# Optimization experiments

Hardware: AMD Instinct MI355X
Metric: run time of the kernel (lower is better)

The kernel has to match this reference:

```python
import jax, jax.numpy as jnp
import numpy as np

B, N, C = 16, 1025, 1024
H, D = 16, 64          # num_heads, head_dim
NPT = 1                # num_prefix_tokens
EPS = 1e-6
SCALE = D ** -0.5


def layer_norm(x, g, b, eps=EPS):
    mu = jnp.mean(x, axis=-1, keepdims=True)
    var = jnp.mean(jnp.square(x - mu), axis=-1, keepdims=True)
    return (x - mu) * jax.lax.rsqrt(var + eps) * g + b


def rot(x):
    # interleaved rotate-half: out[..., ::2] = -x[..., 1::2]; out[..., 1::2] = x[..., ::2]
    x2 = x.reshape(*x.shape[:-1], -1, 2)
    return jnp.stack([-x2[..., 1], x2[..., 0]], axis=-1).reshape(x.shape)


def apply_rot_embed_cat(x, emb):
    # emb: (N_spatial, 2*D) = [sin | cos]
    sin_emb, cos_emb = jnp.split(emb, 2, axis=-1)
    return x * cos_emb + rot(x) * sin_emb


def setup_inputs() -> dict:
    key = jax.random.key(0)
    ks = jax.random.split(key, 12)
    s = 0.02
    return {
        "x": jax.random.normal(ks[0], (B, N, C), jnp.float32),
        "rope": jax.random.normal(ks[1], (N - NPT, 2 * D), jnp.float32),
        "qkv_w": jax.random.normal(ks[2], (3 * C, C), jnp.float32) * s,
        "q_bias": jax.random.normal(ks[3], (C,), jnp.float32) * s,
        "k_bias": jnp.zeros((C,), jnp.float32),  # registered buffer, always zero
        "v_bias": jax.random.normal(ks[4], (C,), jnp.float32) * s,
        "qn_g": jnp.ones((D,), jnp.float32),
        "qn_b": jnp.zeros((D,), jnp.float32),
        "kn_g": jnp.ones((D,), jnp.float32),
        "kn_b": jnp.zeros((D,), jnp.float32),
        "norm_g": jnp.ones((C,), jnp.float32),
        "norm_b": jnp.zeros((C,), jnp.float32),
        "proj_w": jax.random.normal(ks[5], (C, C), jnp.float32) * s,
        "proj_b": jnp.zeros((C,), jnp.float32),
    }


def reference(x, rope, qkv_w, q_bias, k_bias, v_bias, qn_g, qn_b, kn_g, kn_b,
              norm_g, norm_b, proj_w, proj_b):
    b, n, c = x.shape
    qkv_bias = jnp.concatenate([q_bias, k_bias, v_bias])
    qkv = jnp.einsum('bnc,oc->bno', x, qkv_w) + qkv_bias          # (B,N,3C)
    qkv = qkv.reshape(b, n, 3, H, D).transpose(2, 0, 3, 1, 4)     # (3,B,H,N,D)
    q, k, v = qkv[0], qkv[1], qkv[2]
    # per-head QK layernorm over head_dim
    q = layer_norm(q, qn_g, qn_b)
    k = layer_norm(k, kn_g, kn_b)
    # RoPE on spatial tokens only (prefix tokens excluded)
    q = jnp.concatenate([q[:, :, :NPT], apply_rot_embed_cat(q[:, :, NPT:], rope)], axis=2)
    k = jnp.concatenate([k[:, :, :NPT], apply_rot_embed_cat(k[:, :, NPT:], rope)], axis=2)
    # scaled dot product attention
    attn = jnp.einsum('bhqd,bhkd->bhqk', q * SCALE, k)
    attn = jax.nn.softmax(attn, axis=-1)
    out = jnp.einsum('bhqk,bhkd->bhqd', attn, v)                  # (B,H,N,D)
    out = out.transpose(0, 2, 1, 3).reshape(b, n, c)              # (B,N,C)
    out = layer_norm(out, norm_g, norm_b)                         # scale_norm
    out = jnp.einsum('bnc,oc->bno', out, proj_w) + proj_b
    return out
```

## Files before the change

### kernel.cpp

```cpp
#include <hip/hip_runtime.h>
#include <hip/hip_bf16.h>

#define B_ 16
#define N_ 1025
#define C_ 1024
#define H_ 16
#define D_ 64
#define M_ (B_ * N_)
#define EPS_ 1e-6f
#define SCALE_ 0.125f
#define VTS_ 1088

typedef __attribute__((ext_vector_type(8))) short bf16x8;
typedef __attribute__((ext_vector_type(4))) float f32x4;
typedef unsigned short u16;
typedef unsigned int u32;

__device__ inline float bf2f(u16 h) {
    union { u32 u; float f; } c; c.u = ((u32)h) << 16; return c.f;
}
__device__ inline u16 f2bf(float f) {
    union { u32 u; float f; } c; c.f = f;
    u32 r = c.u + 0x7FFF + ((c.u >> 16) & 1);
    return (u16)(r >> 16);
}
__device__ inline u32 cvtpk(float lo, float hi) {
    u32 r;
    asm("v_cvt_pk_bf16_f32 %0, %1, %2" : "=v"(r) : "v"(lo), "v"(hi));
    return r;
}

__device__ inline void gload16(const void* g, void* l) {
    __builtin_amdgcn_global_load_lds(
        (const __attribute__((address_space(1))) void*)g,
        (__attribute__((address_space(3))) void*)l, 16, 0, 0);
}

__global__ void k_sniff(const u32* __restrict__ norm_g_bits, int* __restrict__ flag)
{
    if (threadIdx.x == 0 && blockIdx.x == 0)
        flag[0] = (norm_g_bits[0] == 0x3F800000u) ? 1 : 0;
}

__global__ __launch_bounds__(256) void k_convert(
    const void* __restrict__ src, u16* __restrict__ dst, long n,
    const int* __restrict__ flag)
{
    const int f = flag[0];
    long i0 = ((long)blockIdx.x * 256 + threadIdx.x) * 4;
    long stride = (long)gridDim.x * 1024;
    if (f) {
        const float* s = (const float*)src;
        for (long i = i0; i < n; i += stride) {
#pragma unroll
            for (int j = 0; j < 4; ++j) dst[i + j] = f2bf(s[i + j]);
        }
    } else {
        const u16* s = (const u16*)src;
        for (long i = i0; i < n; i += stride) {
#pragma unroll
            for (int j = 0; j < 4; ++j) dst[i + j] = s[i + j];
        }
    }
}

__global__ __launch_bounds__(256) void k_convert_small(
    const void* s0, const void* s1, const void* s2, const void* s3,
    const void* s4, const void* s5, const void* s6, const void* s7,
    const void* s8, const void* s9, u16* __restrict__ dst,
    const int* __restrict__ flag)
{
    int i = blockIdx.x * 256 + threadIdx.x;
    if (i >= 6400) return;
    const void* src; int off;
    if      (i < 1024) { src = s0; off = i; }
    else if (i < 2048) { src = s1; off = i - 1024; }
    else if (i < 3072) { src = s2; off = i - 2048; }
    else if (i < 3136) { src = s3; off = i - 3072; }
    else if (i < 3200) { src = s4; off = i - 3136; }
    else if (i < 3264) { src = s5; off = i - 3200; }
    else if (i < 3328) { src = s6; off = i - 3264; }
    else if (i < 4352) { src = s7; off = i - 3328; }
    else if (i < 5376) { src = s8; off = i - 4352; }
    else               { src = s9; off = i - 5376; }
    dst[i] = flag[0] ? f2bf(((const float*)src)[off]) : ((const u16*)src)[off];
}

__global__ __launch_bounds__(256) void k_qkv(
    const u16* __restrict__ x, const u16* __restrict__ wmat,
    const u16* __restrict__ qbias, const u16* __restrict__ kbias,
    const u16* __restrict__ vbias,
    u16* __restrict__ q, u16* __restrict__ kk, u16* __restrict__ vv)
{
    __shared__ __attribute__((aligned(16))) u16 As[128 * 32];
    __shared__ __attribute__((aligned(16))) u16 Bs[128 * 32];
    const int t  = threadIdx.x;
    const int m0 = blockIdx.y * 128;
    const int n0 = blockIdx.x * 128;
    const int w  = t >> 6;
    const int ln = t & 15;
    const int qd = (t & 63) >> 4;
    const int wr = (w >> 1) * 64;
    const int wc = (w & 1) * 64;

    f32x4 acc[4][4] = {};

    const int srow = t >> 2;
    const int scol = (t & 3) * 8;
    int ar0 = m0 + srow;       if (ar0 >= M_) ar0 = M_ - 1;
    int ar1 = m0 + 64 + srow;  if (ar1 >= M_) ar1 = M_ - 1;
    const u16* ap0 = x + (size_t)ar0 * C_ + scol;
    const u16* ap1 = x + (size_t)ar1 * C_ + scol;
    const u16* bp0 = wmat + (size_t)(n0 + srow) * C_ + scol;
    const u16* bp1 = wmat + (size_t)(n0 + 64 + srow) * C_ + scol;
    u16* lA0 = &As[t * 8];
    u16* lA1 = &As[2048 + t * 8];
    u16* lB0 = &Bs[t * 8];
    u16* lB1 = &Bs[2048 + t * 8];

    for (int k0 = 0; k0 < C_; k0 += 32) {
        gload16(ap0 + k0, lA0);
        gload16(ap1 + k0, lA1);
        gload16(bp0 + k0, lB0);
        gload16(bp1 + k0, lB1);
        __syncthreads();
        bf16x8 a[4], b[4];
#pragma unroll
        for (int i = 0; i < 4; ++i)
            a[i] = *(const bf16x8*)&As[(wr + i * 16 + ln) * 32 + qd * 8];
#pragma unroll
        for (int j = 0; j < 4; ++j)
            b[j] = *(const bf16x8*)&Bs[(wc + j * 16 + ln) * 32 + qd * 8];
#pragma unroll
        for (int i = 0; i < 4; ++i)
#pragma unroll
            for (int j = 0; j < 4; ++j)
                acc[i][j] = __builtin_amdgcn_mfma_f32_16x16x32_bf16(a[i], b[j], acc[i][j], 0, 0, 0);
        __syncthreads();
    }

#pragma unroll
    for (int j = 0; j < 4; ++j) {
        int o = n0 + wc + j * 16 + ln;
        int part = o >> 10;
        int c = o & 1023;
        int h = c >> 6, d = c & 63;
        const u16* bias = (part == 0) ? qbias : (part == 1) ? kbias : vbias;
        u16* dst = (part == 0) ? q : (part == 1) ? kk : vv;
        float bv = bf2f(bias[c]);
#pragma unroll
        for (int i = 0; i < 4; ++i) {
#pragma unroll
            for (int r = 0; r < 4; ++r) {
                int m = m0 + wr + i * 16 + qd * 4 + r;
                if (m >= M_) continue;
                int bb = m / N_, n = m % N_;
                dst[(((size_t)(bb * H_ + h)) * N_ + n) * D_ + d] = f2bf(acc[i][j][r] + bv);
            }
        }
    }
}

__global__ __launch_bounds__(256) void k_lnrope(
    u16* __restrict__ buf, const u16* __restrict__ g, const u16* __restrict__ bt,
    const u16* __restrict__ rope, float scale)
{
    int wid = (blockIdx.x * 256 + threadIdx.x) >> 6;
    int d = threadIdx.x & 63;
    if (wid >= B_ * H_ * N_) return;
    int n = wid % N_;
    u16* row = buf + (size_t)wid * 64;

    float xv = bf2f(row[d]);
    float s = xv;
#pragma unroll
    for (int off = 32; off; off >>= 1) s += __shfl_xor(s, off);
    float mu = s * (1.f / 64.f);
    float dv = xv - mu;
    float s2 = dv * dv;
#pragma unroll
    for (int off = 32; off; off >>= 1) s2 += __shfl_xor(s2, off);
    float var = s2 * (1.f / 64.f);
    float y = dv * rsqrtf(var + EPS_) * bf2f(g[d]) + bf2f(bt[d]);

    if (n >= 1) {
        const u16* rp = rope + (size_t)(n - 1) * 128;
        float sn = bf2f(rp[d]);
        float cs = bf2f(rp[64 + d]);
        float part = __shfl_xor(y, 1);
        float rot = (d & 1) ? part : -part;
        y = y * cs + rot * sn;
    }
    row[d] = f2bf(y * scale);
}

__global__ __launch_bounds__(256) void k_vt(
    const u16* __restrict__ v, u16* __restrict__ vt)
{
    __shared__ __attribute__((aligned(16))) u16 T[64 * 72];
    const int kb = blockIdx.x % 17;
    const int bh = blockIdx.x / 17;
    const int k0 = kb * 64;
    const size_t src = (size_t)bh * N_ * D_;
    const size_t dst = (size_t)bh * D_ * VTS_;
    const int t = threadIdx.x;

#pragma unroll
    for (int c = 0; c < 2; ++c) {
        int id = c * 256 + t;
        int gk = id >> 3;
        int d0 = (id & 7) * 8;
        int gka = k0 + gk; if (gka > N_ - 1) gka = N_ - 1;
        bf16x8 x = *(const bf16x8*)(v + src + (size_t)gka * D_ + d0);
        int col = d0 ^ (8 * ((gk & 7) ^ (gk >> 3)));
        *(bf16x8*)&T[gk * 72 + col] = x;
    }
    __syncthreads();

#pragma unroll
    for (int c = 0; c < 2; ++c) {
        int id = c * 256 + t;
        int d   = id >> 3;
        int kk0 = (id & 7) * 8;
        bf16x8 pk;
#pragma unroll
        for (int j = 0; j < 8; ++j) {
            int key = kk0 + j;
            int col = d ^ (8 * ((key & 7) ^ (key >> 3)));
            pk[j] = (short)T[key * 72 + col];
        }
        *(bf16x8*)(vt + dst + (size_t)d * VTS_ + k0 + kk0) = pk;
    }
}

__global__ __launch_bounds__(256) void k_attn(
    const u16* __restrict__ q, const u16* __restrict__ k,
    const u16* __restrict__ vt, u16* __restrict__ out)
{
    __shared__ __attribute__((aligned(16))) u16 Ks[64 * 72];
    __shared__ __attribute__((aligned(16))) u16 Vs[64 * 72];
    __shared__ __attribute__((aligned(16))) u16 Pt[4][2][16 * 72];

    const int t  = threadIdx.x;
    const int w  = t >> 6;
    const int ln = t & 15;
    const int qd = (t & 63) >> 4;

    const int p  = blockIdx.x;
    const int g  = (p & 7) + 8 * ((p >> 3) / 9);
    const int qb = (p >> 3) % 9;
    const int b = g >> 4, h = g & 15;
    const size_t kbase = (size_t)g * N_ * D_;
    const size_t vbase = (size_t)g * D_ * VTS_;
    const int qw = qb * 128 + w * 32;

    bf16x8 qa[2][2];
#pragma unroll
    for (int a = 0; a < 2; ++a) {
        int row = qw + a * 16 + ln; if (row > N_ - 1) row = N_ - 1;
        const u16* qp = q + kbase + (size_t)row * D_;
        qa[a][0] = *(const bf16x8*)(qp + qd * 8);
        qa[a][1] = *(const bf16x8*)(qp + 32 + qd * 8);
    }

    f32x4 o_acc[2][4] = {};
    float m_run[2] = { -1e30f, -1e30f };
    float l_run[2] = { 0.f, 0.f };
    const f32x4 zf = { 0.f, 0.f, 0.f, 0.f };

    const int skey = t >> 3;
    const int sdg  = t & 7;

    bf16x8 pk[2], pv[2];
#pragma unroll
    for (int c = 0; c < 2; ++c) {
        int r32 = c * 32 + skey;
        pk[c] = *(const bf16x8*)(k + kbase + (size_t)r32 * D_ + sdg * 8);
        pv[c] = *(const bf16x8*)(vt + vbase + (size_t)r32 * VTS_ + sdg * 8);
    }

    for (int k0 = 0; k0 < N_; k0 += 64) {
#pragma unroll
        for (int c = 0; c < 2; ++c) {
            int r32 = c * 32 + skey;
            *(bf16x8*)&Ks[r32 * 72 + sdg * 8] = pk[c];
            *(bf16x8*)&Vs[r32 * 72 + sdg * 8] = pv[c];
        }
        __syncthreads();

        const int k1 = k0 + 64;
        if (k1 < N_) {
#pragma unroll
            for (int c = 0; c < 2; ++c) {
                int r32 = c * 32 + skey;
                int gk = k1 + r32; if (gk > N_ - 1) gk = N_ - 1;
                pk[c] = *(const bf16x8*)(k + kbase + (size_t)gk * D_ + sdg * 8);
                pv[c] = *(const bf16x8*)(vt + vbase + (size_t)r32 * VTS_ + k1 + sdg * 8);
            }
        }

        bf16x8 kf[4][2];
#pragma unroll
        for (int ks = 0; ks < 4; ++ks) {
            kf[ks][0] = *(const bf16x8*)&Ks[(ks * 16 + ln) * 72 + qd * 8];
            kf[ks][1] = *(const bf16x8*)&Ks[(ks * 16 + ln) * 72 + 32 + qd * 8];
        }

        f32x4 s2[2][4];
        __builtin_amdgcn_s_setprio(1);
#pragma unroll
        for (int a = 0; a < 2; ++a)
#pragma unroll
            for (int ks = 0; ks < 4; ++ks) {
                s2[a][ks] = __builtin_amdgcn_mfma_f32_16x16x32_bf16(kf[ks][0], qa[a][0], zf, 0, 0, 0);
                s2[a][ks] = __builtin_amdgcn_mfma_f32_16x16x32_bf16(kf[ks][1], qa[a][1], s2[a][ks], 0, 0, 0);
            }
        __builtin_amdgcn_s_setprio(0);

        if (k0 + 64 > N_) {
#pragma unroll
            for (int a = 0; a < 2; ++a)
#pragma unroll
                for (int ks = 0; ks < 4; ++ks)
#pragma unroll
                    for (int r = 0; r < 4; ++r)
                        if (k0 + 16 * ks + 4 * qd + r > N_ - 1) s2[a][ks][r] = -1e30f;
        }

        float mx[2];
#pragma unroll
        for (int a = 0; a < 2; ++a) {
            float t0 = fmaxf(fmaxf(s2[a][0][0], s2[a][0][1]), fmaxf(s2[a][0][2], s2[a][0][3]));
            float t1 = fmaxf(fmaxf(s2[a][1][0], s2[a][1][1]), fmaxf(s2[a][1][2], s2[a][1][3]));
            float t2 = fmaxf(fmaxf(s2[a][2][0], s2[a][2][1]), fmaxf(s2[a][2][2], s2[a][2][3]));
            float t3 = fmaxf(fmaxf(s2[a][3][0], s2[a][3][1]), fmaxf(s2[a][3][2], s2[a][3][3]));
            float m = fmaxf(fmaxf(t0, t1), fmaxf(t2, t3));
            m = fmaxf(m, __shfl_xor(m, 16));
            m = fmaxf(m, __shfl_xor(m, 32));
            mx[a] = m;
        }

#pragma unroll
        for (int a = 0; a < 2; ++a) {
            if (__any(mx[a] > m_run[a])) {
                float mn = fmaxf(m_run[a], mx[a]);
                float al = __expf(m_run[a] - mn);
                m_run[a] = mn;
                l_run[a] *= al;
#pragma unroll
                for (int nt = 0; nt < 4; ++nt)
#pragma unroll
                    for (int r = 0; r < 4; ++r)
                        o_acc[a][nt][r] *= al;
            }
            const float mcur = m_run[a];
            float rs = 0.f;
#pragma unroll
            for (int ks = 0; ks < 4; ++ks)
#pragma unroll
                for (int r = 0; r < 4; ++r) {
                    s2[a][ks][r] = __expf(s2[a][ks][r] - mcur);
                    rs += s2[a][ks][r];
                }
            rs += __shfl_xor(rs, 16);
            rs += __shfl_xor(rs, 32);
            l_run[a] += rs;

            u16* pt = &Pt[w][a][0];
#pragma unroll
            for (int ks = 0; ks < 4; ++ks) {
                *(u32*)&pt[ln * 72 + 16 * ks + 4 * qd]     = cvtpk(s2[a][ks][0], s2[a][ks][1]);
                *(u32*)&pt[ln * 72 + 16 * ks + 4 * qd + 2] = cvtpk(s2[a][ks][2], s2[a][ks][3]);
            }
        }

        bf16x8 pf[2][2];
#pragma unroll
        for (int a = 0; a < 2; ++a) {
            const u16* pt = &Pt[w][a][0];
            pf[a][0] = *(const bf16x8*)&pt[ln * 72 + qd * 8];
            pf[a][1] = *(const bf16x8*)&pt[ln * 72 + 32 + qd * 8];
        }

        __builtin_amdgcn_s_setprio(1);
#pragma unroll
        for (int nt = 0; nt < 4; ++nt) {
            bf16x8 v0 = *(const bf16x8*)&Vs[(nt * 16 + ln) * 72 + qd * 8];
            bf16x8 v1 = *(const bf16x8*)&Vs[(nt * 16 + ln) * 72 + 32 + qd * 8];
#pragma unroll
            for (int a = 0; a < 2; ++a) {
                o_acc[a][nt] = __builtin_amdgcn_mfma_f32_16x16x32_bf16(v0, pf[a][0], o_acc[a][nt], 0, 0, 0);
                o_acc[a][nt] = __builtin_amdgcn_mfma_f32_16x16x32_bf16(v1, pf[a][1], o_acc[a][nt], 0, 0, 0);
            }
        }
        __builtin_amdgcn_s_setprio(0);
        __syncthreads();
    }

#pragma unroll
    for (int a = 0; a < 2; ++a) {
        int n = qw + a * 16 + ln;
        if (n >= N_) continue;
        float lr = l_run[a];
        u16* op = out + ((size_t)b * N_ + n) * C_ + h * 64;
#pragma unroll
        for (int nt = 0; nt < 4; ++nt)
#pragma unroll
            for (int rp = 0; rp < 2; ++rp) {
                int d = nt * 16 + qd * 4 + rp * 2;
                *(u32*)&op[d] = cvtpk(o_acc[a][nt][rp * 2] / lr,
                                      o_acc[a][nt][rp * 2 + 1] / lr);
            }
    }
}

__global__ __launch_bounds__(256) void k_ln(
    const u16* __restrict__ in, const u16* __restrict__ g,
    const u16* __restrict__ bt, u16* __restrict__ outb)
{
    __shared__ float red[8];
    const int row = blockIdx.x;
    const int t = threadIdx.x;
    const u16* p = in + (size_t)row * C_;

    float vals[4];
    float s = 0.f;
#pragma unroll
    for (int i = 0; i < 4; ++i) { vals[i] = bf2f(p[t + i * 256]); s += vals[i]; }
#pragma unroll
    for (int off = 32; off; off >>= 1) s += __shfl_xor(s, off);
    if ((t & 63) == 0) red[t >> 6] = s;
    __syncthreads();
    float mu = (red[0] + red[1] + red[2] + red[3]) * (1.f / 1024.f);
    float s2 = 0.f;
#pragma unroll
    for (int i = 0; i < 4; ++i) { float d = vals[i] - mu; s2 += d * d; }
#pragma unroll
    for (int off = 32; off; off >>= 1) s2 += __shfl_xor(s2, off);
    __syncthreads();
    if ((t & 63) == 0) red[t >> 6] = s2;
    __syncthreads();
    float var = (red[0] + red[1] + red[2] + red[3]) * (1.f / 1024.f);
    float rs = rsqrtf(var + EPS_);
#pragma unroll
    for (int i = 0; i < 4; ++i) {
        int cidx = t + i * 256;
        float y = (vals[i] - mu) * rs * bf2f(g[cidx]) + bf2f(bt[cidx]);
        outb[(size_t)row * C_ + cidx] = f2bf(y);
    }
}

__global__ __launch_bounds__(256) void k_proj(
    const u16* __restrict__ y, const u16* __restrict__ wmat,
    const u16* __restrict__ bias, void* __restrict__ out,
    const int* __restrict__ flag)
{
    __shared__ __attribute__((aligned(16))) u16 As[128 * 32];
    __shared__ __attribute__((aligned(16))) u16 Bs[128 * 32];
    const int t  = threadIdx.x;
    const int m0 = blockIdx.y * 128;
    const int n0 = blockIdx.x * 128;
    const int w  = t >> 6;
    const int ln = t & 15;
    const int qd = (t & 63) >> 4;
    const int wr = (w >> 1) * 64;
    const int wc = (w & 1) * 64;

    f32x4 acc[4][4] = {};

    const int srow = t >> 2;
    const int scol = (t & 3) * 8;
    int ar0 = m0 + srow;       if (ar0 >= M_) ar0 = M_ - 1;
    int ar1 = m0 + 64 + srow;  if (ar1 >= M_) ar1 = M_ - 1;
    const u16* ap0 = y + (size_t)ar0 * C_ + scol;
    const u16* ap1 = y + (size_t)ar1 * C_ + scol;
    const u16* bp0 = wmat + (size_t)(n0 + srow) * C_ + scol;
    const u16* bp1 = wmat + (size_t)(n0 + 64 + srow) * C_ + scol;
    u16* lA0 = &As[t * 8];
    u16* lA1 = &As[2048 + t * 8];
    u16* lB0 = &Bs[t * 8];
    u16* lB1 = &Bs[2048 + t * 8];

    for (int k0 = 0; k0 < C_; k0 += 32) {
        gload16(ap0 + k0, lA0);
        gload16(ap1 + k0, lA1);
        gload16(bp0 + k0, lB0);
        gload16(bp1 + k0, lB1);
        __syncthreads();
        bf16x8 a[4], b[4];
#pragma unroll
        for (int i = 0; i < 4; ++i)
            a[i] = *(const bf16x8*)&As[(wr + i * 16 + ln) * 32 + qd * 8];
#pragma unroll
        for (int j = 0; j < 4; ++j)
            b[j] = *(const bf16x8*)&Bs[(wc + j * 16 + ln) * 32 + qd * 8];
#pragma unroll
        for (int i = 0; i < 4; ++i)
#pragma unroll
            for (int j = 0; j < 4; ++j)
                acc[i][j] = __builtin_amdgcn_mfma_f32_16x16x32_bf16(a[i], b[j], acc[i][j], 0, 0, 0);
        __syncthreads();
    }

    const int f32out = flag[0];
#pragma unroll
    for (int j = 0; j < 4; ++j) {
        int o = n0 + wc + j * 16 + ln;
        float bv = bf2f(bias[o]);
#pragma unroll
        for (int i = 0; i < 4; ++i) {
#pragma unroll
            for (int r = 0; r < 4; ++r) {
                int m = m0 + wr + i * 16 + qd * 4 + r;
                if (m >= M_) continue;
                float val = acc[i][j][r] + bv;
                if (f32out) ((float*)out)[(size_t)m * C_ + o] = val;
                else        ((u16*)out)[(size_t)m * C_ + o] = f2bf(val);
            }
        }
    }
}

extern "C" void kernel_launch(void* const* d_in, const int* in_sizes, int n_in,
                              void* d_out, int out_size, void* d_ws, size_t ws_size,
                              hipStream_t stream)
{
    char* ws = (char*)d_ws;
    int* flag = (int*)ws;
    u16* arena = (u16*)(ws + 256);

    const long X_OFF = 0,            X_N = (long)M_ * C_;
    const long R_OFF = X_OFF + X_N,  R_N = (long)(N_ - 1) * 2 * D_;
    const long W_OFF = R_OFF + R_N,  W_N = (long)3 * C_ * C_;
    const long P_OFF = W_OFF + W_N,  P_N = (long)C_ * C_;
    const long S_OFF = P_OFF + P_N;
    const long ARENA_N = S_OFF + 6400;

    u16* xb   = arena + X_OFF;
    u16* ropb = arena + R_OFF;
    u16* qkvw = arena + W_OFF;
    u16* pw   = arena + P_OFF;
    u16* qb   = arena + S_OFF;
    u16* kb   = qb + 1024;
    u16* vb   = kb + 1024;
    u16* qng  = vb + 1024;
    u16* qnb  = qng + 64;
    u16* kng  = qnb + 64;
    u16* knb  = kng + 64;
    u16* ng   = knb + 64;
    u16* nb   = ng + 1024;
    u16* pb   = nb + 1024;

    char* after = (char*)(arena + ARENA_N);
    const size_t sz = (size_t)B_ * H_ * N_ * D_ * 2;
    u16* qbuf = (u16*)after;
    u16* kbuf = (u16*)(after + sz);
    u16* vbuf = (u16*)(after + 2 * sz);
    u16* vtb  = (u16*)(after + 3 * sz);
    u16* ao   = xb;
    u16* ybuf = qbuf;

    k_sniff<<<1, 64, 0, stream>>>((const u32*)d_in[10], flag);

    k_convert<<<4096, 256, 0, stream>>>(d_in[0], xb, X_N, flag);
    k_convert<<<128, 256, 0, stream>>>(d_in[1], ropb, R_N, flag);
    k_convert<<<2048, 256, 0, stream>>>(d_in[2], qkvw, W_N, flag);
    k_convert<<<1024, 256, 0, stream>>>(d_in[12], pw, P_N, flag);
    k_convert_small<<<25, 256, 0, stream>>>(
        d_in[3], d_in[4], d_in[5], d_in[6], d_in[7], d_in[8], d_in[9],
        d_in[10], d_in[11], d_in[13], qb, flag);

    dim3 g1(24, 129);
    k_qkv<<<g1, 256, 0, stream>>>(xb, qkvw, qb, kb, vb, qbuf, kbuf, vbuf);

    const int rows = B_ * H_ * N_;
    k_lnrope<<<(rows + 3) / 4, 256, 0, stream>>>(qbuf, qng, qnb, ropb, SCALE_);
    k_lnrope<<<(rows + 3) / 4, 256, 0, stream>>>(kbuf, kng, knb, ropb, 1.0f);

    k_vt<<<B_ * H_ * 17, 256, 0, stream>>>(vbuf, vtb);

    k_attn<<<B_ * H_ * 9, 256, 0, stream>>>(qbuf, kbuf, vtb, ao);

    k_ln<<<M_, 256, 0, stream>>>(ao, ng, nb, ybuf);

    dim3 g2(8, 129);
    k_proj<<<g2, 256, 0, stream>>>(ybuf, pw, pb, d_out, flag);
}
```

Measured before the change: 670.8 us.

## Stage GEMM and attention epilogues through LDS, remap grids, widen attention blocks

The QKV GEMM epilogue now writes each tile through shared memory and stores 16-byte vectors, replacing scattered 2-byte stores into the head-major Q/K/V buffers. The attention output path is restaged the same way. Both GEMMs switch to a 1D grid with an XCD-aware block remap to improve L2 locality. Attention blocks grow to 9 waves covering 288 queries, so each K/V tile load is shared by more queries, while only 8 waves do the loads. The cost is more LDS traffic and bigger blocks that may lower occupancy.

Result: faster. 627.7 us (-6.4%).

```diff
diff --git a/kernel.cpp b/kernel.cpp
--- a/kernel.cpp
+++ b/kernel.cpp
@@ -13,6 +13,7 @@
 
 typedef __attribute__((ext_vector_type(8))) short bf16x8;
 typedef __attribute__((ext_vector_type(4))) float f32x4;
+typedef __attribute__((ext_vector_type(2))) unsigned int u32x2;
 typedef unsigned short u16;
 typedef unsigned int u32;
 
@@ -95,8 +96,10 @@
     __shared__ __attribute__((aligned(16))) u16 As[128 * 32];
     __shared__ __attribute__((aligned(16))) u16 Bs[128 * 32];
     const int t  = threadIdx.x;
-    const int m0 = blockIdx.y * 128;
-    const int n0 = blockIdx.x * 128;
+    const int bid = blockIdx.x;
+    const int wg = (bid & 7) * 387 + (bid >> 3);
+    const int m0 = (wg / 24) * 128;
+    const int n0 = (wg % 24) * 128;
     const int w  = t >> 6;
     const int ln = t & 15;
     const int qd = (t & 63) >> 4;
@@ -139,24 +142,33 @@
         __syncthreads();
     }
 
-#pragma unroll
-    for (int j = 0; j < 4; ++j) {
-        int o = n0 + wc + j * 16 + ln;
-        int part = o >> 10;
-        int c = o & 1023;
-        int h = c >> 6, d = c & 63;
-        const u16* bias = (part == 0) ? qbias : (part == 1) ? kbias : vbias;
-        u16* dst = (part == 0) ? q : (part == 1) ? kk : vv;
-        float bv = bf2f(bias[c]);
-#pragma unroll
-        for (int i = 0; i < 4; ++i) {
-#pragma unroll
-            for (int r = 0; r < 4; ++r) {
-                int m = m0 + wr + i * 16 + qd * 4 + r;
-                if (m >= M_) continue;
-                int bb = m / N_, n = m % N_;
-                dst[(((size_t)(bb * H_ + h)) * N_ + n) * D_ + d] = f2bf(acc[i][j][r] + bv);
-            }
+    u16* Ts = (w == 3) ? Bs : &As[w * 1152];
+    const int obase = n0 + wc;
+    const int part = obase >> 10;
+    const int c0 = obase & 1023;
+    const int hh = c0 >> 6;
+    const u16* bias = (part == 0) ? qbias : (part == 1) ? kbias : vbias;
+    u16* dst = (part == 0) ? q : (part == 1) ? kk : vv;
+    const int lrow = (t & 63) >> 2;
+    const int lchk = t & 3;
+#pragma unroll
+    for (int i = 0; i < 4; ++i) {
+#pragma unroll
+        for (int j = 0; j < 4; ++j) {
+            float bv = bf2f(bias[c0 + j * 16 + ln]);
+#pragma unroll
+            for (int r = 0; r < 4; ++r)
+                Ts[(qd * 4 + r) * 72 + j * 16 + ln] = f2bf(acc[i][j][r] + bv);
+        }
+        int m = m0 + wr + i * 16 + lrow;
+        if (m < M_) {
+            int bb = m / N_;
+            int n = m - bb * N_;
+            bf16x8 x0 = *(const bf16x8*)&Ts[lrow * 72 + lchk * 16];
+            bf16x8 x1 = *(const bf16x8*)&Ts[lrow * 72 + lchk * 16 + 8];
+            u16* dp = dst + (((size_t)(bb * H_ + hh)) * N_ + n) * D_ + lchk * 16;
+            *(bf16x8*)dp = x0;
+            *(bf16x8*)(dp + 8) = x1;
         }
     }
 }
@@ -233,26 +245,27 @@
     }
 }
 
-__global__ __launch_bounds__(256) void k_attn(
+__global__ __launch_bounds__(576) void k_attn(
     const u16* __restrict__ q, const u16* __restrict__ k,
     const u16* __restrict__ vt, u16* __restrict__ out)
 {
     __shared__ __attribute__((aligned(16))) u16 Ks[64 * 72];
     __shared__ __attribute__((aligned(16))) u16 Vs[64 * 72];
-    __shared__ __attribute__((aligned(16))) u16 Pt[4][2][16 * 72];
+    __shared__ __attribute__((aligned(16))) u16 Pt[9][2][16 * 72];
 
     const int t  = threadIdx.x;
     const int w  = t >> 6;
+    const int l  = t & 63;
     const int ln = t & 15;
-    const int qd = (t & 63) >> 4;
+    const int qd = l >> 4;
 
     const int p  = blockIdx.x;
-    const int g  = (p & 7) + 8 * ((p >> 3) / 9);
-    const int qb = (p >> 3) % 9;
+    const int g  = (p & 7) + 8 * ((p >> 3) >> 2);
+    const int qt = (p >> 3) & 3;
     const int b = g >> 4, h = g & 15;
     const size_t kbase = (size_t)g * N_ * D_;
     const size_t vbase = (size_t)g * D_ * VTS_;
-    const int qw = qb * 128 + w * 32;
+    const int qw = qt * 288 + w * 32;
 
     bf16x8 qa[2][2];
 #pragma unroll
@@ -271,32 +284,24 @@
     const int skey = t >> 3;
     const int sdg  = t & 7;
 
-    bf16x8 pk[2], pv[2];
-#pragma unroll
-    for (int c = 0; c < 2; ++c) {
-        int r32 = c * 32 + skey;
-        pk[c] = *(const bf16x8*)(k + kbase + (size_t)r32 * D_ + sdg * 8);
-        pv[c] = *(const bf16x8*)(vt + vbase + (size_t)r32 * VTS_ + sdg * 8);
+    bf16x8 pk = {}, pv = {};
+    if (w < 8) {
+        pk = *(const bf16x8*)(k + kbase + (size_t)skey * D_ + sdg * 8);
+        pv = *(const bf16x8*)(vt + vbase + (size_t)skey * VTS_ + sdg * 8);
     }
 
     for (int k0 = 0; k0 < N_; k0 += 64) {
-#pragma unroll
-        for (int c = 0; c < 2; ++c) {
-            int r32 = c * 32 + skey;
-            *(bf16x8*)&Ks[r32 * 72 + sdg * 8] = pk[c];
-            *(bf16x8*)&Vs[r32 * 72 + sdg * 8] = pv[c];
+        if (w < 8) {
+            *(bf16x8*)&Ks[skey * 72 + sdg * 8] = pk;
+            *(bf16x8*)&Vs[skey * 72 + sdg * 8] = pv;
         }
         __syncthreads();
 
         const int k1 = k0 + 64;
-        if (k1 < N_) {
-#pragma unroll
-            for (int c = 0; c < 2; ++c) {
-                int r32 = c * 32 + skey;
-                int gk = k1 + r32; if (gk > N_ - 1) gk = N_ - 1;
-                pk[c] = *(const bf16x8*)(k + kbase + (size_t)gk * D_ + sdg * 8);
-                pv[c] = *(const bf16x8*)(vt + vbase + (size_t)r32 * VTS_ + k1 + sdg * 8);
-            }
+        if (w < 8 && k1 < N_) {
+            int gk = k1 + skey; if (gk > N_ - 1) gk = N_ - 1;
+            pk = *(const bf16x8*)(k + kbase + (size_t)gk * D_ + sdg * 8);
+            pv = *(const bf16x8*)(vt + vbase + (size_t)skey * VTS_ + k1 + sdg * 8);
         }
 
         bf16x8 kf[4][2];
@@ -369,8 +374,10 @@
             u16* pt = &Pt[w][a][0];
 #pragma unroll
             for (int ks = 0; ks < 4; ++ks) {
-                *(u32*)&pt[ln * 72 + 16 * ks + 4 * qd]     = cvtpk(s2[a][ks][0], s2[a][ks][1]);
-                *(u32*)&pt[ln * 72 + 16 * ks + 4 * qd + 2] = cvtpk(s2[a][ks][2], s2[a][ks][3]);
+                u32x2 pr;
+                pr.x = cvtpk(s2[a][ks][0], s2[a][ks][1]);
+                pr.y = cvtpk(s2[a][ks][2], s2[a][ks][3]);
+                *(u32x2*)&pt[ln * 72 + 16 * ks + 4 * qd] = pr;
             }
         }
 
@@ -399,18 +406,24 @@
 
 #pragma unroll
     for (int a = 0; a < 2; ++a) {
-        int n = qw + a * 16 + ln;
-        if (n >= N_) continue;
         float lr = l_run[a];
-        u16* op = out + ((size_t)b * N_ + n) * C_ + h * 64;
-#pragma unroll
-        for (int nt = 0; nt < 4; ++nt)
-#pragma unroll
-            for (int rp = 0; rp < 2; ++rp) {
-                int d = nt * 16 + qd * 4 + rp * 2;
-                *(u32*)&op[d] = cvtpk(o_acc[a][nt][rp * 2] / lr,
-                                      o_acc[a][nt][rp * 2 + 1] / lr);
-            }
+        u16* pt = &Pt[w][a][0];
+#pragma unroll
+        for (int nt = 0; nt < 4; ++nt) {
+            u32x2 pr;
+            pr.x = cvtpk(o_acc[a][nt][0] / lr, o_acc[a][nt][1] / lr);
+            pr.y = cvtpk(o_acc[a][nt][2] / lr, o_acc[a][nt][3] / lr);
+            *(u32x2*)&pt[ln * 72 + nt * 16 + qd * 4] = pr;
+        }
+        int row = l >> 2, chunk = l & 3;
+        int n = qw + a * 16 + row;
+        if (n < N_) {
+            bf16x8 x0 = *(const bf16x8*)&pt[row * 72 + chunk * 16];
+            bf16x8 x1 = *(const bf16x8*)&pt[row * 72 + chunk * 16 + 8];
+            u16* op = out + ((size_t)b * N_ + n) * C_ + h * 64 + chunk * 16;
+            *(bf16x8*)op = x0;
+            *(bf16x8*)(op + 8) = x1;
+        }
     }
 }
 
@@ -458,8 +471,10 @@
     __shared__ __attribute__((aligned(16))) u16 As[128 * 32];
     __shared__ __attribute__((aligned(16))) u16 Bs[128 * 32];
     const int t  = threadIdx.x;
-    const int m0 = blockIdx.y * 128;
-    const int n0 = blockIdx.x * 128;
+    const int bid = blockIdx.x;
+    const int wg = (bid & 7) * 129 + (bid >> 3);
+    const int m0 = (wg >> 3) * 128;
+    const int n0 = (wg & 7) * 128;
     const int w  = t >> 6;
     const int ln = t & 15;
     const int qd = (t & 63) >> 4;
@@ -570,8 +585,7 @@
         d_in[3], d_in[4], d_in[5], d_in[6], d_in[7], d_in[8], d_in[9],
         d_in[10], d_in[11], d_in[13], qb, flag);
 
-    dim3 g1(24, 129);
-    k_qkv<<<g1, 256, 0, stream>>>(xb, qkvw, qb, kb, vb, qbuf, kbuf, vbuf);
+    k_qkv<<<3096, 256, 0, stream>>>(xb, qkvw, qb, kb, vb, qbuf, kbuf, vbuf);
 
     const int rows = B_ * H_ * N_;
     k_lnrope<<<(rows + 3) / 4, 256, 0, stream>>>(qbuf, qng, qnb, ropb, SCALE_);
@@ -579,10 +593,9 @@
 
     k_vt<<<B_ * H_ * 17, 256, 0, stream>>>(vbuf, vtb);
 
-    k_attn<<<B_ * H_ * 9, 256, 0, stream>>>(qbuf, kbuf, vtb, ao);
+    k_attn<<<B_ * H_ * 4, 576, 0, stream>>>(qbuf, kbuf, vtb, ao);
 
     k_ln<<<M_, 256, 0, stream>>>(ao, ng, nb, ybuf);
 
-    dim3 g2(8, 129);
-    k_proj<<<g2, 256, 0, stream>>>(ybuf, pw, pb, d_out, flag);
-}
+    k_proj<<<1032, 256, 0, stream>>>(ybuf, pw, pb, d_out, flag);
+}
```
